# Performance work log

Measured on AMD Instinct MI355X. Metric: run time of the kernel, lower is better.

The kernel has to match this reference:

```python
import jax, jax.numpy as jnp
import numpy as np

SIZE = 5
DIM = 64


def setup_inputs() -> dict:
    key = jax.random.key(0)
    k0, k1, k2, k3, k4 = jax.random.split(key, 5)
    bs, C, H, W = 4, 3, 1024, 1024
    x = jax.random.uniform(k0, (bs, C, H, W), dtype=jnp.float32)
    n_off = SIZE * SIZE
    # conv1x1_{i}_E: Conv2d(1, DIM, 1) -> weight (DIM,1,1,1) ~= vector (DIM,), bias (DIM,)
    # conv1x1_{i}_S: Conv2d(DIM, 1, 1) -> weight (1,DIM,1,1) ~= vector (DIM,), bias ()
    wE = jax.random.normal(k1, (n_off, DIM), dtype=jnp.float32)            # fan_in=1 -> U(-1,1)-ish scale
    bE = jax.random.normal(k2, (n_off, DIM), dtype=jnp.float32) * 0.5
    wS = jax.random.normal(k3, (n_off, DIM), dtype=jnp.float32) * (1.0 / np.sqrt(DIM))
    bS = jax.random.normal(k4, (n_off,), dtype=jnp.float32) * 0.1
    return {"x": x, "wE": wE, "bE": bE, "wS": wS, "bS": bS}


def reference(x, wE, bE, wS, bS):
    size = SIZE
    pad = size // 2
    bs, C, H, W = x.shape
    xc = jnp.clip(x, 0.0, 1.0).reshape(bs * C, H, W)            # (N,H,W)
    xp = jnp.pad(xc, ((0, 0), (pad, pad), (pad, pad)), mode="reflect")
    # 25 shifted views, stacked: (K, N, H, W). Small fixed python loop over offsets.
    shifts = jnp.stack([xp[:, i:i + H, j:j + W]
                        for i in range(size) for j in range(size)])
    # Per offset k, S(E(x)) is linear in x (no nonlinearity between the 1x1 convs):
    #   out_k = (wS_k . wE_k) * x_k + (wS_k . bE_k + bS_k)
    a = jnp.einsum("kd,kd->k", wS, wE)                          # per-offset scale
    c = jnp.einsum("kd,kd->k", wS, bE) + bS                     # per-offset pixel-constant bias
    out = jnp.einsum("k,knhw->nhw", a, shifts) + c.sum()
    out = out / (size * size)
    out = jnp.clip(out, 0.0, 1.0)
    return out.reshape(bs, C, H, W)
```

## Files before the change

### kernel.cpp

```cpp
#include <hip/hip_runtime.h>
#include <hip/hip_bf16.h>


#define HH 1024
#define WW 1024
#define NIMG 12
#define TBH 16
#define ROWS (TBH + 4)
#define PF 8

typedef float f32x4 __attribute__((ext_vector_type(4)));
typedef float f32x2 __attribute__((ext_vector_type(2)));

__device__ __forceinline__ float readlane_f(float v, int lane) {
    return __int_as_float(__builtin_amdgcn_readlane(__float_as_int(v), lane));
}

__device__ __forceinline__ float sgpr_bcast(float v) {
    return __int_as_float(__builtin_amdgcn_readfirstlane(__float_as_int(v)));
}

__device__ __forceinline__ float dot4(f32x4 a, f32x4 b) {
    return a.x * b.x + a.y * b.y + a.z * b.z + a.w * b.w;
}

__device__ __forceinline__ f32x4 clip01v4(f32x4 v) {
    f32x4 z = {0.f, 0.f, 0.f, 0.f};
    f32x4 o = {1.f, 1.f, 1.f, 1.f};
    return __builtin_elementwise_min(__builtin_elementwise_max(v, z), o);
}

__device__ __forceinline__ f32x2 clip01v2(f32x2 v) {
    f32x2 z = {0.f, 0.f};
    f32x2 o = {1.f, 1.f};
    return __builtin_elementwise_min(__builtin_elementwise_max(v, z), o);
}

__global__ __launch_bounds__(256) void conv5_kernel(const float* __restrict__ x,
                                                    const float* __restrict__ wE,
                                                    const float* __restrict__ bE,
                                                    const float* __restrict__ wS,
                                                    const float* __restrict__ bS,
                                                    float* __restrict__ out) {
    int lane = threadIdx.x & 63;

    float apass[2], cacc = 0.f;
    #pragma unroll
    for (int p = 0; p < 2; ++p) {
        int k = p * 16 + (lane >> 2);
        float a = 0.f;
        if (k < 25) {
            int base = k * 64 + (lane & 3) * 16;
            #pragma unroll
            for (int i = 0; i < 4; ++i) {
                f32x4 sv = *(const f32x4*)(wS + base + 4 * i);
                f32x4 ev = *(const f32x4*)(wE + base + 4 * i);
                f32x4 bv = *(const f32x4*)(bE + base + 4 * i);
                a += dot4(sv, ev);
                cacc += dot4(sv, bv);
            }
        }
        a += __shfl_xor(a, 1);
        a += __shfl_xor(a, 2);
        apass[p] = a;
    }
    if (lane < 25) cacc += bS[lane];
    #pragma unroll
    for (int off = 32; off; off >>= 1) cacc += __shfl_xor(cacc, off);
    float bias = sgpr_bcast(cacc * (1.f / 25.f));
    f32x2 bias2 = {bias, bias};

    float wv[25];
    #pragma unroll
    for (int k = 0; k < 16; ++k) wv[k] = readlane_f(apass[0], 4 * k) * (1.f / 25.f);
    #pragma unroll
    for (int k = 16; k < 25; ++k) wv[k] = readlane_f(apass[1], 4 * (k - 16)) * (1.f / 25.f);

    int nwg = gridDim.x;
    int cpx = nwg >> 3;
    int l = (blockIdx.x & 7) * cpx + (blockIdx.x >> 3);
    int img = l >> 6;
    int rb = l & 63;
    int row0 = rb * TBH;

    const float* src = x + (size_t)img * (HH * WW);
    int tid = threadIdx.x;
    int cbase = tid * 4;

    bool lt = (cbase == 0);
    bool rt = (cbase == 1020);
    int qa = lt ? 0 : cbase - 2;
    int qb = rt ? 1020 : cbase + 2;

    auto rowptr = [&](int ir) -> const float* {
        int prow = row0 - 2 + ir;
        int sr = prow < 0 ? -prow : (prow >= HH ? 2 * HH - 2 - prow : prow);
        return src + (size_t)sr * WW;
    };

    f32x4 bufA[PF], bufB[PF];
    f32x2 acc[5][2];

    #pragma unroll
    for (int ir = 0; ir < PF; ++ir) {
        const float* rp = rowptr(ir);
        bufA[ir] = *(const f32x4*)(rp + qa);
        bufB[ir] = *(const f32x4*)(rp + qb);
    }
    __builtin_amdgcn_sched_barrier(0);

    float* op = out + (size_t)img * (HH * WW) + (size_t)row0 * WW + cbase;

    #pragma unroll
    for (int ir = 0; ir < ROWS; ++ir) {
        f32x4 A = bufA[ir & (PF - 1)];
        f32x4 B = bufB[ir & (PF - 1)];
        if (ir + PF < ROWS) {
            const float* rp = rowptr(ir + PF);
            bufA[ir & (PF - 1)] = *(const f32x4*)(rp + qa);
            bufB[ir & (PF - 1)] = *(const f32x4*)(rp + qb);
        }

        A = clip01v4(A);
        B = clip01v4(B);

        float r8[8] = {A.x, A.y, A.z, A.w, B.x, B.y, B.z, B.w};
        r8[0] = lt ? A.z : r8[0];
        r8[2] = lt ? A.x : r8[2];
        r8[3] = lt ? A.y : r8[3];
        r8[4] = rt ? B.z : r8[4];
        r8[5] = rt ? B.w : r8[5];
        r8[7] = rt ? B.y : r8[7];

        f32x2 pr[7];
        #pragma unroll
        for (int j = 0; j < 7; ++j) { pr[j].x = r8[j]; pr[j].y = r8[j + 1]; }

        if (ir < TBH) {
            acc[ir % 5][0] = bias2;
            acc[ir % 5][1] = bias2;
        }

        #pragma unroll
        for (int dr = 0; dr < 5; ++dr) {
            int orow = ir - dr;
            if (orow < 0 || orow >= TBH) continue;
            #pragma unroll
            for (int j = 0; j < 5; ++j) {
                float wj = wv[dr * 5 + j];
                f32x2 w2 = {wj, wj};
                acc[orow % 5][0] += pr[j] * w2;
                acc[orow % 5][1] += pr[j + 2] * w2;
            }
        }

        if (ir >= 4) {
            int orow = ir - 4;
            f32x2 lo = clip01v2(acc[orow % 5][0]);
            f32x2 hi = clip01v2(acc[orow % 5][1]);
            f32x4 o = {lo.x, lo.y, hi.x, hi.y};
            *(f32x4*)(op + (size_t)orow * WW) = o;
        }
    }
}

extern "C" void kernel_launch(void* const* d_in, const int* in_sizes, int n_in,
                              void* d_out, int out_size, void* d_ws, size_t ws_size,
                              hipStream_t stream) {
    const float* x  = (const float*)d_in[0];
    const float* wE = (const float*)d_in[1];
    const float* bE = (const float*)d_in[2];
    const float* wS = (const float*)d_in[3];
    const float* bS = (const float*)d_in[4];
    float* out = (float*)d_out;

    int nblocks = NIMG * (HH / TBH);
    conv5_kernel<<<nblocks, 256, 0, stream>>>(x, wE, bE, wS, bS, out);
}
```

Baseline: 24.51 us.

## Stage input rows into LDS via global_load_lds with explicit vmcnt pipelining

Replaces the per-thread overlapping register loads (two 16-byte loads per row with a 4-wide halo) with direct global-to-LDS loads: one 16-byte load per lane plus a 4-byte tail load that supplies the halo, into an 8-slot per-wave ring buffer. Each row is then read back from LDS as two overlapping vectors. Manual s_waitcnt vmcnt values control a prefetch depth of 6 rows. The aim is to cut redundant global traffic and VGPR pressure, at the cost of LDS round trips and fragile hand-set wait counts. Edge reflection is done through the tail-offset choice and an LDS fixup written by lane 0.

```diff
diff --git a/kernel.cpp b/kernel.cpp
--- a/kernel.cpp
+++ b/kernel.cpp
@@ -7,7 +7,9 @@
 #define NIMG 12
 #define TBH 16
 #define ROWS (TBH + 4)
-#define PF 8
+#define PF 6
+#define SLOTB 1280
+#define NSLOT 8
 
 typedef float f32x4 __attribute__((ext_vector_type(4)));
 typedef float f32x2 __attribute__((ext_vector_type(2)));
@@ -15,26 +17,24 @@
 __device__ __forceinline__ float readlane_f(float v, int lane) {
     return __int_as_float(__builtin_amdgcn_readlane(__float_as_int(v), lane));
 }
-
 __device__ __forceinline__ float sgpr_bcast(float v) {
     return __int_as_float(__builtin_amdgcn_readfirstlane(__float_as_int(v)));
 }
-
 __device__ __forceinline__ float dot4(f32x4 a, f32x4 b) {
     return a.x * b.x + a.y * b.y + a.z * b.z + a.w * b.w;
 }
-
 __device__ __forceinline__ f32x4 clip01v4(f32x4 v) {
     f32x4 z = {0.f, 0.f, 0.f, 0.f};
     f32x4 o = {1.f, 1.f, 1.f, 1.f};
     return __builtin_elementwise_min(__builtin_elementwise_max(v, z), o);
 }
-
 __device__ __forceinline__ f32x2 clip01v2(f32x2 v) {
     f32x2 z = {0.f, 0.f};
     f32x2 o = {1.f, 1.f};
     return __builtin_elementwise_min(__builtin_elementwise_max(v, z), o);
 }
+
+#define VMWAIT(n) asm volatile("s_waitcnt vmcnt(" #n ")" ::: "memory")
 
 __global__ __launch_bounds__(256) void conv5_kernel(const float* __restrict__ x,
                                                     const float* __restrict__ wE,
@@ -42,7 +42,11 @@
                                                     const float* __restrict__ wS,
                                                     const float* __restrict__ bS,
                                                     float* __restrict__ out) {
-    int lane = threadIdx.x & 63;
+    int tid  = threadIdx.x;
+    int lane = tid & 63;
+    int wave = tid >> 6;
+
+    __shared__ __align__(16) char lds[4 * NSLOT * SLOTB];
 
     float apass[2], cacc = 0.f;
     #pragma unroll
@@ -84,13 +88,20 @@
     int row0 = rb * TBH;
 
     const float* src = x + (size_t)img * (HH * WW);
-    int tid = threadIdx.x;
-    int cbase = tid * 4;
+    int s = wave << 8;
+    int cbase = s + 4 * lane;
+    bool img_lt = (s == 0);
+    bool img_rt = (s + 256 == WW);
 
-    bool lt = (cbase == 0);
-    bool rt = (cbase == 1020);
-    int qa = lt ? 0 : cbase - 2;
-    int qb = rt ? 1020 : cbase + 2;
+    int coff_main = (img_lt && lane == 0) ? 0 : (s - 2 + 4 * lane);
+    int coff_tail;
+    if (img_rt) coff_tail = (lane == 1) ? 1023 : ((lane == 3) ? 1021 : 1022);
+    else {
+        coff_tail = s + 254 + lane;
+        if (coff_tail > WW - 1) coff_tail = WW - 1;
+    }
+
+    char* lwbase = lds + wave * (NSLOT * SLOTB);
 
     auto rowptr = [&](int ir) -> const float* {
         int prow = row0 - 2 + ir;
@@ -98,70 +109,67 @@
         return src + (size_t)sr * WW;
     };
 
-    f32x4 bufA[PF], bufB[PF];
+    auto stage = [&](int r) {
+        const float* rp = rowptr(r);
+        char* lb = lwbase + (r & (NSLOT - 1)) * SLOTB;
+        __builtin_amdgcn_global_load_lds((const float*)(rp + coff_main),
+                                         (float*)lb, 16, 0, 0);
+        __builtin_amdgcn_global_load_lds((const float*)(rp + coff_tail),
+                                         (float*)(lb + 1024), 4, 0, 0);
+    };
+
     f32x2 acc[5][2];
-
-    #pragma unroll
-    for (int ir = 0; ir < PF; ++ir) {
-        const float* rp = rowptr(ir);
-        bufA[ir] = *(const f32x4*)(rp + qa);
-        bufB[ir] = *(const f32x4*)(rp + qb);
-    }
-    __builtin_amdgcn_sched_barrier(0);
-
     float* op = out + (size_t)img * (HH * WW) + (size_t)row0 * WW + cbase;
 
     #pragma unroll
-    for (int ir = 0; ir < ROWS; ++ir) {
-        f32x4 A = bufA[ir & (PF - 1)];
-        f32x4 B = bufB[ir & (PF - 1)];
-        if (ir + PF < ROWS) {
-            const float* rp = rowptr(ir + PF);
-            bufA[ir & (PF - 1)] = *(const f32x4*)(rp + qa);
-            bufB[ir & (PF - 1)] = *(const f32x4*)(rp + qb);
-        }
+    for (int r = 0; r < PF; ++r) stage(r);
 
-        A = clip01v4(A);
-        B = clip01v4(B);
+#define BODY(ir, vn) {                                                        \
+    if ((ir) + PF < ROWS) stage((ir) + PF);                                   \
+    VMWAIT(vn);                                                               \
+    __builtin_amdgcn_sched_barrier(0);                                        \
+    char* lb = lwbase + ((ir) & (NSLOT - 1)) * SLOTB;                         \
+    if (img_lt && lane == 0) {           \
+        f32x4 t = *(f32x4*)lb;                        \
+        f32x4 w4 = {t.z, t.y, t.x, t.y};                \
+        *(f32x4*)lb = w4;                                                     \
+    }                                                                         \
+    f32x4 u = *(f32x4*)(lb + 16 * lane);                                      \
+    f32x4 v = *(f32x4*)(lb + 16 * lane + 16);                                 \
+    u = clip01v4(u);                                                          \
+    v = clip01v4(v);                                                          \
+    float r8[8] = {u.x, u.y, u.z, u.w, v.x, v.y, v.z, v.w};                   \
+    f32x2 pr[7];                                                              \
+    _Pragma("unroll")                                                         \
+    for (int j = 0; j < 7; ++j) { pr[j].x = r8[j]; pr[j].y = r8[j + 1]; }     \
+    if ((ir) < TBH) { acc[(ir) % 5][0] = bias2; acc[(ir) % 5][1] = bias2; }   \
+    _Pragma("unroll")                                                         \
+    for (int dr = 0; dr < 5; ++dr) {                                          \
+        int orow = (ir) - dr;                                                 \
+        if (orow >= 0 && orow < TBH) {                                        \
+            _Pragma("unroll")                                                 \
+            for (int j = 0; j < 5; ++j) {                                     \
+                float wj = wv[dr * 5 + j];                                    \
+                f32x2 w2 = {wj, wj};                                          \
+                acc[orow % 5][0] += pr[j] * w2;                               \
+                acc[orow % 5][1] += pr[j + 2] * w2;                           \
+            }                                                                 \
+        }                                                                     \
+    }                                                                         \
+    if ((ir) >= 4) {                                                          \
+        int orow = (ir) - 4;                                                  \
+        f32x2 lo = clip01v2(acc[orow % 5][0]);                                \
+        f32x2 hi = clip01v2(acc[orow % 5][1]);                                \
+        f32x4 o = {lo.x, lo.y, hi.x, hi.y};                                   \
+        *(f32x4*)(op + (size_t)orow * WW) = o;                                \
+    }                                                                         \
+}
 
-        float r8[8] = {A.x, A.y, A.z, A.w, B.x, B.y, B.z, B.w};
-        r8[0] = lt ? A.z : r8[0];
-        r8[2] = lt ? A.x : r8[2];
-        r8[3] = lt ? A.y : r8[3];
-        r8[4] = rt ? B.z : r8[4];
-        r8[5] = rt ? B.w : r8[5];
-        r8[7] = rt ? B.y : r8[7];
-
-        f32x2 pr[7];
-        #pragma unroll
-        for (int j = 0; j < 7; ++j) { pr[j].x = r8[j]; pr[j].y = r8[j + 1]; }
-
-        if (ir < TBH) {
-            acc[ir % 5][0] = bias2;
-            acc[ir % 5][1] = bias2;
-        }
-
-        #pragma unroll
-        for (int dr = 0; dr < 5; ++dr) {
-            int orow = ir - dr;
-            if (orow < 0 || orow >= TBH) continue;
-            #pragma unroll
-            for (int j = 0; j < 5; ++j) {
-                float wj = wv[dr * 5 + j];
-                f32x2 w2 = {wj, wj};
-                acc[orow % 5][0] += pr[j] * w2;
-                acc[orow % 5][1] += pr[j + 2] * w2;
-            }
-        }
-
-        if (ir >= 4) {
-            int orow = ir - 4;
-            f32x2 lo = clip01v2(acc[orow % 5][0]);
-            f32x2 hi = clip01v2(acc[orow % 5][1]);
-            f32x4 o = {lo.x, lo.y, hi.x, hi.y};
-            *(f32x4*)(op + (size_t)orow * WW) = o;
-        }
-    }
+    BODY(0, 12)  BODY(1, 12)  BODY(2, 12)  BODY(3, 12)  BODY(4, 12)
+    BODY(5, 12)  BODY(6, 12)  BODY(7, 12)  BODY(8, 12)  BODY(9, 12)
+    BODY(10, 12) BODY(11, 12) BODY(12, 12) BODY(13, 12) BODY(14, 10)
+    BODY(15, 8)  BODY(16, 6)  BODY(17, 4)  BODY(18, 2)  BODY(19, 0)
+#undef BODY
 }
 
 extern "C" void kernel_launch(void* const* d_in, const int* in_sizes, int n_in,
```

Result: no change. 24.55 us (+0.1%).
